# Kernel tuning notes

Measured on AMD Instinct MI355X. Metric: run time of the kernel, lower is better.

## Reference

```python
import jax, jax.numpy as jnp
import numpy as np

N = 50000      # nodes
E = 800000     # edges
F = 500        # num_features
HID = 64       # hidden_channels
H = 4          # num_heads
HC = HID // H  # headc = 16
C = 8          # num_classes
KHOP = 2       # K hops
CST = 1e-5


def setup_inputs() -> dict:
    key = jax.random.key(0)
    ks = jax.random.split(key, 12)
    s = 0.02
    return {
        "node_feat": jax.random.normal(ks[0], (N, F), dtype=jnp.float32),
        "edge_index": jax.random.randint(ks[1], (2, E), 0, N, dtype=jnp.int64),
        "Wi": jax.random.normal(ks[2], (F, HID), dtype=jnp.float32) * s,
        "bi": jnp.zeros((HID,), dtype=jnp.float32),
        "Wq": jax.random.normal(ks[3], (HID, H * HC), dtype=jnp.float32) * s,
        "bq": jnp.zeros((H * HC,), dtype=jnp.float32),
        "Wk": jax.random.normal(ks[4], (HID, H * HC), dtype=jnp.float32) * s,
        "bk": jnp.zeros((H * HC,), dtype=jnp.float32),
        "Wv": jax.random.normal(ks[5], (HID, H * C), dtype=jnp.float32) * s,
        "bv": jnp.zeros((H * C,), dtype=jnp.float32),
        "Wo": jax.random.normal(ks[6], (H * C, C), dtype=jnp.float32) * s,
        "bo": jnp.zeros((C,), dtype=jnp.float32),
        "hopwise": jnp.ones((KHOP + 1,), dtype=jnp.float32),
        "headwise": jnp.zeros((H, KHOP), dtype=jnp.float32),
        "teleport": jnp.ones((1,), dtype=jnp.float32),
    }


def reference(node_feat, edge_index, Wi, bi, Wq, bq, Wk, bk, Wv, bv, Wo, bo,
              hopwise, headwise, teleport):
    row, col = edge_index[0], edge_index[1]
    # degree(col): in-degree; norm = deg^-1 indexed at row (as in the torch code)
    deg = jax.ops.segment_sum(jnp.ones((E,), dtype=node_feat.dtype), col,
                              num_segments=N)
    deg_inv = jnp.where(deg > 0, 1.0 / deg, 0.0)  # [N]

    x = jax.nn.relu(node_feat @ Wi + bi)          # dropout p=0.0 / eval -> identity
    Q = (1.0 + jax.nn.elu(x @ Wq + bq)).reshape(N, H, HC)
    Kf = (1.0 + jax.nn.elu(x @ Wk + bk)).reshape(N, H, HC)
    V = (x @ Wv + bv).reshape(N, H, C)

    M = jnp.einsum('nhi,nhj->nhij', Kf, V)        # [N,H,HC,C]
    hidden = V * hopwise[0]                       # ind_gamma & gamma_softmax
    layerwise = jax.nn.softmax(headwise, axis=0)  # softmax over heads (dim=-2)

    # global attention (teleport) term
    teleportM = jnp.sum(M, axis=0, keepdims=True) / N      # [1,H,HC,C]
    teleportK = jnp.sum(Kf, axis=0, keepdims=True) / N     # [1,H,HC]
    teleportH = jnp.einsum('nhi,bhij->nhj', Q, teleportM)  # [N,H,C]
    teleportC = jnp.einsum('nhi,bhi->nh', Q, teleportK)[..., None] + CST
    teleportH = (teleportH / teleportC).sum(axis=-2)       # [N,C]

    for hop in range(KHOP):
        # norm[e] = deg_inv[row[e]]  =>  pre-scale source nodes, then scatter-add
        M = jax.ops.segment_sum((M * deg_inv[:, None, None, None])[row], col,
                                num_segments=N)
        Kf = jax.ops.segment_sum((Kf * deg_inv[:, None, None])[row], col,
                                 num_segments=N)
        Hh = jnp.einsum('nhi,nhij->nhj', Q, M)             # [N,H,C]
        Cc = jnp.einsum('nhi,nhi->nh', Q, Kf)[..., None] + CST
        gamma = hopwise[hop + 1] * layerwise[:, hop][:, None]  # [H,1]
        hidden = hidden + gamma * (Hh / Cc)

    # multi_concat output projection
    hidden = hidden.reshape(N, H * C) @ Wo + bo
    return hidden + teleport * teleportH
```

## Files before the change

### kernel.cpp

```cpp
#include <hip/hip_runtime.h>
#include <hip/hip_bf16.h>
#include <stdint.h>
#include <stddef.h>

#define NN 50000
#define NE 800000
#define FIN 500
#define HIDN 64
#define NH 4
#define HCD 16
#define NC 8
#define KVROW 192
#define SROW 640
#define CSTF 1e-5f
#define SCAN_NB 196

typedef float f32x2 __attribute__((ext_vector_type(2)));
typedef __attribute__((ext_vector_type(8))) short bf16x8;
typedef __attribute__((ext_vector_type(4))) float f32x4;

__device__ inline float bf_lo(unsigned u) {
    union { unsigned i; float f; } v; v.i = u << 16; return v.f;
}
__device__ inline float bf_hi(unsigned u) {
    union { unsigned i; float f; } v; v.i = u & 0xffff0000u; return v.f;
}
__device__ inline unsigned short f2bf(float f) {
    union { float f; unsigned i; } v; v.f = f;
    unsigned r = v.i + 0x7fffu + ((v.i >> 16) & 1u);
    return (unsigned short)(r >> 16);
}


__global__ void k_deg(const int* __restrict__ col, int* __restrict__ deg) {
    int e = blockIdx.x * blockDim.x + threadIdx.x;
    if (e < NE) atomicAdd(&deg[col[e]], 1);
}

__global__ void k_deginv(const int* __restrict__ deg, float* __restrict__ dinv,
                         int* __restrict__ cursor) {
    int i = blockIdx.x * blockDim.x + threadIdx.x;
    if (i < NN) {
        dinv[i] = deg[i] > 0 ? 1.0f / (float)deg[i] : 0.0f;
        cursor[i] = 0;
    }
}

__global__ void k_bsum(const int* __restrict__ deg, int* __restrict__ bsum) {
    __shared__ int red[256];
    int b = blockIdx.x, t = threadIdx.x;
    int i = b * 256 + t;
    red[t] = (i < NN) ? deg[i] : 0;
    __syncthreads();
    for (int d = 128; d > 0; d >>= 1) {
        if (t < d) red[t] += red[t + d];
        __syncthreads();
    }
    if (t == 0) bsum[b] = red[0];
}

__global__ void k_bscan(const int* __restrict__ bsum, int* __restrict__ bex) {
    __shared__ int s[256];
    int t = threadIdx.x;
    int own = (t < SCAN_NB) ? bsum[t] : 0;
    s[t] = own;
    __syncthreads();
    for (int d = 1; d < 256; d <<= 1) {
        int v = (t >= d) ? s[t - d] : 0;
        __syncthreads();
        s[t] += v;
        __syncthreads();
    }
    if (t < SCAN_NB) bex[t] = s[t] - own;
}

__global__ void k_expand(const int* __restrict__ deg, const int* __restrict__ bex,
                         int* __restrict__ offs) {
    __shared__ int s[256];
    int b = blockIdx.x, t = threadIdx.x;
    int i = b * 256 + t;
    int v = (i < NN) ? deg[i] : 0;
    s[t] = v;
    __syncthreads();
    for (int d = 1; d < 256; d <<= 1) {
        int a = (t >= d) ? s[t - d] : 0;
        __syncthreads();
        s[t] += a;
        __syncthreads();
    }
    int excl = s[t] - v + bex[b];
    if (i < NN) offs[i] = excl;
    if (i == NN - 1) offs[NN] = excl + v;
}

__global__ void k_scatter(const int* __restrict__ row, const int* __restrict__ col,
                          const int* __restrict__ offs, int* __restrict__ cursor,
                          int* __restrict__ csr_src) {
    int e = blockIdx.x * blockDim.x + threadIdx.x;
    if (e < NE) {
        int c = col[e];
        int pos = offs[c] + atomicAdd(&cursor[c], 1);
        csr_src[pos] = row[e];
    }
}


__global__ __launch_bounds__(256) void k_xgemm(const float* __restrict__ nf,
                                               const float* __restrict__ Wi,
                                               const float* __restrict__ bi,
                                               float* __restrict__ x) {
    __shared__ __align__(16) unsigned short a_s[64 * 40];
    __shared__ __align__(16) unsigned short w_s[64 * 40];
    int t = threadIdx.x;
    int lane = t & 63;
    int w = t >> 6;
    int quad = lane >> 4;
    int l15 = lane & 15;
    int n0 = blockIdx.x * 64;

    f32x4 acc[4];
#pragma unroll
    for (int ct = 0; ct < 4; ct++) acc[ct] = (f32x4){0.f, 0.f, 0.f, 0.f};

    for (int k0 = 0; k0 < FIN; k0 += 32) {
        __syncthreads();
#pragma unroll
        for (int p = 0; p < 2; p++) {
            int i = t + p * 256;
            int row = i >> 3;
            int k4 = (i & 7) * 4;
            int kk = k0 + k4;
            int n = n0 + row;
            float4 v = make_float4(0.f, 0.f, 0.f, 0.f);
            if (n < NN && kk < FIN)
                v = *(const float4*)&nf[(size_t)n * FIN + kk];
            unsigned short* d = &a_s[row * 40 + k4];
            d[0] = f2bf(v.x); d[1] = f2bf(v.y); d[2] = f2bf(v.z); d[3] = f2bf(v.w);
        }
#pragma unroll
        for (int p = 0; p < 2; p++) {
            int i = t + p * 256;
            int krow = i >> 4;
            int c4 = (i & 15) * 4;
            int kk = k0 + krow;
            float4 v = make_float4(0.f, 0.f, 0.f, 0.f);
            if (kk < FIN)
                v = *(const float4*)&Wi[(size_t)kk * 64 + c4];
            w_s[(c4 + 0) * 40 + krow] = f2bf(v.x);
            w_s[(c4 + 1) * 40 + krow] = f2bf(v.y);
            w_s[(c4 + 2) * 40 + krow] = f2bf(v.z);
            w_s[(c4 + 3) * 40 + krow] = f2bf(v.w);
        }
        __syncthreads();
        bf16x8 af = *(const bf16x8*)&a_s[(w * 16 + l15) * 40 + quad * 8];
#pragma unroll
        for (int ct = 0; ct < 4; ct++) {
            bf16x8 bf = *(const bf16x8*)&w_s[(ct * 16 + l15) * 40 + quad * 8];
            acc[ct] = __builtin_amdgcn_mfma_f32_16x16x32_bf16(af, bf, acc[ct], 0, 0, 0);
        }
    }
#pragma unroll
    for (int ct = 0; ct < 4; ct++) {
        int c = ct * 16 + l15;
        float bv = bi[c];
#pragma unroll
        for (int r = 0; r < 4; r++) {
            int n = n0 + w * 16 + quad * 4 + r;
            if (n < NN)
                x[(size_t)n * 64 + c] = fmaxf(acc[ct][r] + bv, 0.f);
        }
    }
}


__global__ __launch_bounds__(256) void k_qkv(const float* __restrict__ x,
    const float* __restrict__ Wq, const float* __restrict__ bq,
    const float* __restrict__ Wk, const float* __restrict__ bk,
    const float* __restrict__ Wv, const float* __restrict__ bv,
    const float* __restrict__ hopwise, const float* __restrict__ dinv,
    float* __restrict__ Qg, float* __restrict__ hid,
    unsigned char* __restrict__ kv0, float* __restrict__ tMK) {
    __shared__ float wq_s[64 * 64], wk_s[64 * 64], wv_s[64 * 32];
    __shared__ float bq_s[64], bk_s[64], bv_s[32];
    __shared__ float xs[4][8][64];
    __shared__ float tacc[576];
    int t = threadIdx.x;
    for (int i = t; i < 4096; i += 256) { wq_s[i] = Wq[i]; wk_s[i] = Wk[i]; }
    for (int i = t; i < 2048; i += 256) wv_s[i] = Wv[i];
    if (t < 64) { bq_s[t] = bq[t]; bk_s[t] = bk[t]; }
    if (t >= 64 && t < 96) bv_s[t - 64] = bv[t - 64];
    for (int i = t; i < 576; i += 256) tacc[i] = 0.f;
    __syncthreads();
    int lane = t & 63;
    int w = t >> 6;
    int h = lane >> 4;
    int vcol = lane & 31;
    float hw0 = hopwise[0];
    float tkp = 0.f;
    float tmp_[8];
#pragma unroll
    for (int j = 0; j < 8; j++) tmp_[j] = 0.f;
    int tiles = (NN + 31) >> 5;
    for (int tile = blockIdx.x; tile < tiles; tile += gridDim.x) {
        int n0 = tile * 32 + w * 8;
        __syncthreads();
#pragma unroll
        for (int u = 0; u < 8; u++) {
            int n = n0 + u;
            xs[w][u][lane] = (n < NN) ? x[(size_t)n * 64 + lane] : 0.f;
        }
        __syncthreads();
        float aq[8], ak[8], av[8];
#pragma unroll
        for (int u = 0; u < 8; u++) { aq[u] = 0.f; ak[u] = 0.f; av[u] = 0.f; }
        for (int f = 0; f < 64; f++) {
            float wqv = wq_s[f * 64 + lane];
            float wkv = wk_s[f * 64 + lane];
            float wvv = wv_s[f * 32 + vcol];
#pragma unroll
            for (int u = 0; u < 8; u++) {
                float xf = xs[w][u][f];
                aq[u] = fmaf(xf, wqv, aq[u]);
                ak[u] = fmaf(xf, wkv, ak[u]);
                av[u] = fmaf(xf, wvv, av[u]);
            }
        }
#pragma unroll
        for (int u = 0; u < 8; u++) {
            int n = n0 + u;
            float q = aq[u] + bq_s[lane];
            float k = ak[u] + bk_s[lane];
            float v = av[u] + bv_s[vcol];
            float Qv = q > 0.f ? 1.f + q : expf(q);
            float Kv = k > 0.f ? 1.f + k : expf(k);
            if (n < NN) {
                Qg[(size_t)n * 64 + lane] = Qv;
                float vj[8];
#pragma unroll
                for (int j = 0; j < 8; j++) vj[j] = __shfl(v, h * 8 + j, 64);
                tkp += Kv;
#pragma unroll
                for (int j = 0; j < 8; j++) tmp_[j] += Kv * vj[j];
                float dv = dinv[n];
                unsigned short* kvrow = (unsigned short*)(kv0 + (size_t)n * KVROW);
                kvrow[lane] = f2bf(Kv * dv);
                if (lane < 32) kvrow[64 + lane] = f2bf(v);
                if (lane < 32) hid[(size_t)n * 32 + lane] = v * hw0;
            }
        }
    }
#pragma unroll
    for (int j = 0; j < 8; j++) atomicAdd(&tacc[lane * 8 + j], tmp_[j]);
    atomicAdd(&tacc[512 + lane], tkp);
    __syncthreads();
    for (int i = t; i < 576; i += 256) atomicAdd(&tMK[i], tacc[i]);
}


__global__ __launch_bounds__(256) void k_hop0(const unsigned char* __restrict__ kv0,
    const int* __restrict__ offs, const int* __restrict__ csr_src,
    const float* __restrict__ dinv, const float* __restrict__ Qg,
    const float* __restrict__ hopwise, const float* __restrict__ headwise,
    unsigned char* __restrict__ S1, float* __restrict__ hid) {
    int t = threadIdx.x;
    int lane = t & 63;
    int n = (blockIdx.x * 256 + t) >> 6;
    if (n >= NN) return;
    int h = lane >> 4;
    float e0 = expf(headwise[0 * 2 + 0]);
    float e1 = expf(headwise[1 * 2 + 0]);
    float e2 = expf(headwise[2 * 2 + 0]);
    float e3 = expf(headwise[3 * 2 + 0]);
    float esum = e0 + e1 + e2 + e3;
    float eh = (h == 0) ? e0 : ((h == 1) ? e1 : ((h == 2) ? e2 : e3));
    float gam = hopwise[1] * eh / esum;

    int hoff = 128 + h * 16;
    int o0 = offs[n], o1 = offs[n + 1];
    float kacc = 0.f;
    float4 m0 = make_float4(0.f, 0.f, 0.f, 0.f);
    float4 m1 = make_float4(0.f, 0.f, 0.f, 0.f);
    int e = o0;
    for (; e + 1 < o1; e += 2) {
        int sa = csr_src[e];
        int sb = csr_src[e + 1];
        const unsigned char* ra = kv0 + (size_t)sa * KVROW;
        const unsigned char* rb = kv0 + (size_t)sb * KVROW;
        float ka = bf_lo(((const unsigned short*)ra)[lane]);
        uint4 va = *(const uint4*)(ra + hoff);
        float kb = bf_lo(((const unsigned short*)rb)[lane]);
        uint4 vb = *(const uint4*)(rb + hoff);
        kacc += ka;
        m0.x = fmaf(ka, bf_lo(va.x), m0.x); m0.y = fmaf(ka, bf_hi(va.x), m0.y);
        m0.z = fmaf(ka, bf_lo(va.y), m0.z); m0.w = fmaf(ka, bf_hi(va.y), m0.w);
        m1.x = fmaf(ka, bf_lo(va.z), m1.x); m1.y = fmaf(ka, bf_hi(va.z), m1.y);
        m1.z = fmaf(ka, bf_lo(va.w), m1.z); m1.w = fmaf(ka, bf_hi(va.w), m1.w);
        kacc += kb;
        m0.x = fmaf(kb, bf_lo(vb.x), m0.x); m0.y = fmaf(kb, bf_hi(vb.x), m0.y);
        m0.z = fmaf(kb, bf_lo(vb.y), m0.z); m0.w = fmaf(kb, bf_hi(vb.y), m0.w);
        m1.x = fmaf(kb, bf_lo(vb.z), m1.x); m1.y = fmaf(kb, bf_hi(vb.z), m1.y);
        m1.z = fmaf(kb, bf_lo(vb.w), m1.z); m1.w = fmaf(kb, bf_hi(vb.w), m1.w);
    }
    if (e < o1) {
        int sa = csr_src[e];
        const unsigned char* ra = kv0 + (size_t)sa * KVROW;
        float ka = bf_lo(((const unsigned short*)ra)[lane]);
        uint4 va = *(const uint4*)(ra + hoff);
        kacc += ka;
        m0.x = fmaf(ka, bf_lo(va.x), m0.x); m0.y = fmaf(ka, bf_hi(va.x), m0.y);
        m0.z = fmaf(ka, bf_lo(va.y), m0.z); m0.w = fmaf(ka, bf_hi(va.y), m0.w);
        m1.x = fmaf(ka, bf_lo(va.z), m1.x); m1.y = fmaf(ka, bf_hi(va.z), m1.y);
        m1.z = fmaf(ka, bf_lo(va.w), m1.w); m1.w = fmaf(ka, bf_hi(va.w), m1.w);
    }
    {
        float dv = dinv[n];
        float s16 = dv * 16.f;
        unsigned char* drow = S1 + (size_t)n * SROW;
        ((unsigned short*)drow)[lane] = f2bf(kacc * dv);
        unsigned u0 = __builtin_amdgcn_cvt_pk_fp8_f32(m0.x * s16, m0.y * s16, 0, false);
        u0 = __builtin_amdgcn_cvt_pk_fp8_f32(m0.z * s16, m0.w * s16, u0, true);
        unsigned u1 = __builtin_amdgcn_cvt_pk_fp8_f32(m1.x * s16, m1.y * s16, 0, false);
        u1 = __builtin_amdgcn_cvt_pk_fp8_f32(m1.z * s16, m1.w * s16, u1, true);
        uint2 pv; pv.x = u0; pv.y = u1;
        *(uint2*)(drow + 128 + lane * 8) = pv;
    }
    float qv = Qg[(size_t)n * 64 + lane];
    float hh[8];
    hh[0] = qv * m0.x; hh[1] = qv * m0.y; hh[2] = qv * m0.z; hh[3] = qv * m0.w;
    hh[4] = qv * m1.x; hh[5] = qv * m1.y; hh[6] = qv * m1.z; hh[7] = qv * m1.w;
    float cc = qv * kacc;
#pragma unroll
    for (int s = 1; s < 16; s <<= 1) {
#pragma unroll
        for (int j = 0; j < 8; j++) hh[j] += __shfl_xor(hh[j], s, 16);
        cc += __shfl_xor(cc, s, 16);
    }
    if ((lane & 15) < 8) {
        int j = lane & 7;
        float val = j < 4 ? (j < 2 ? (j == 0 ? hh[0] : hh[1]) : (j == 2 ? hh[2] : hh[3]))
                          : (j < 6 ? (j == 4 ? hh[4] : hh[5]) : (j == 6 ? hh[6] : hh[7]));
        size_t idx = (size_t)n * 32 + h * 8 + j;
        hid[idx] += gam * val / (cc + CSTF);
    }
}


__global__ __launch_bounds__(256) void k_prop1(const unsigned char* __restrict__ Sold,
    const int* __restrict__ offs, const int* __restrict__ csr_src,
    const float* __restrict__ Qg, const float* __restrict__ hopwise,
    const float* __restrict__ headwise, float* __restrict__ hid) {
    int t = threadIdx.x;
    int lane = t & 63;
    int n = (blockIdx.x * 256 + t) >> 6;
    if (n >= NN) return;
    int h = lane >> 4;
    float e0 = expf(headwise[0 * 2 + 1]);
    float e1 = expf(headwise[1 * 2 + 1]);
    float e2 = expf(headwise[2 * 2 + 1]);
    float e3 = expf(headwise[3 * 2 + 1]);
    float esum = e0 + e1 + e2 + e3;
    float eh = (h == 0) ? e0 : ((h == 1) ? e1 : ((h == 2) ? e2 : e3));
    float gam = hopwise[2] * eh / esum * 0.0625f;

    int o0 = offs[n], o1 = offs[n + 1];
    float kacc = 0.f;
    float4 m0 = make_float4(0.f, 0.f, 0.f, 0.f);
    float4 m1 = make_float4(0.f, 0.f, 0.f, 0.f);
    int e = o0;
    for (; e + 1 < o1; e += 2) {
        int sa = csr_src[e];
        int sb = csr_src[e + 1];
        const unsigned char* ra = Sold + (size_t)sa * SROW;
        const unsigned char* rb = Sold + (size_t)sb * SROW;
        float ka = bf_lo(((const unsigned short*)ra)[lane]);
        uint2 mva = *(const uint2*)(ra + 128 + lane * 8);
        float kb = bf_lo(((const unsigned short*)rb)[lane]);
        uint2 mvb = *(const uint2*)(rb + 128 + lane * 8);
        kacc += ka;
        {
            f32x2 a0 = __builtin_amdgcn_cvt_pk_f32_fp8(mva.x, false);
            f32x2 a1 = __builtin_amdgcn_cvt_pk_f32_fp8(mva.x, true);
            f32x2 b0 = __builtin_amdgcn_cvt_pk_f32_fp8(mva.y, false);
            f32x2 b1 = __builtin_amdgcn_cvt_pk_f32_fp8(mva.y, true);
            m0.x += a0.x; m0.y += a0.y; m0.z += a1.x; m0.w += a1.y;
            m1.x += b0.x; m1.y += b0.y; m1.z += b1.x; m1.w += b1.y;
        }
        kacc += kb;
        {
            f32x2 a0 = __builtin_amdgcn_cvt_pk_f32_fp8(mvb.x, false);
            f32x2 a1 = __builtin_amdgcn_cvt_pk_f32_fp8(mvb.x, true);
            f32x2 b0 = __builtin_amdgcn_cvt_pk_f32_fp8(mvb.y, false);
            f32x2 b1 = __builtin_amdgcn_cvt_pk_f32_fp8(mvb.y, true);
            m0.x += a0.x; m0.y += a0.y; m0.z += a1.x; m0.w += a1.y;
            m1.x += b0.x; m1.y += b0.y; m1.z += b1.x; m1.w += b1.y;
        }
    }
    if (e < o1) {
        int sa = csr_src[e];
        const unsigned char* ra = Sold + (size_t)sa * SROW;
        float ka = bf_lo(((const unsigned short*)ra)[lane]);
        uint2 mva = *(const uint2*)(ra + 128 + lane * 8);
        kacc += ka;
        f32x2 a0 = __builtin_amdgcn_cvt_pk_f32_fp8(mva.x, false);
        f32x2 a1 = __builtin_amdgcn_cvt_pk_f32_fp8(mva.x, true);
        f32x2 b0 = __builtin_amdgcn_cvt_pk_f32_fp8(mva.y, false);
        f32x2 b1 = __builtin_amdgcn_cvt_pk_f32_fp8(mva.y, true);
        m0.x += a0.x; m0.y += a0.y; m0.z += a1.x; m0.w += a1.y;
        m1.x += b0.x; m1.y += b0.y; m1.z += b1.x; m1.w += b1.y;
    }
    float qv = Qg[(size_t)n * 64 + lane];
    float hh[8];
    hh[0] = qv * m0.x; hh[1] = qv * m0.y; hh[2] = qv * m0.z; hh[3] = qv * m0.w;
    hh[4] = qv * m1.x; hh[5] = qv * m1.y; hh[6] = qv * m1.z; hh[7] = qv * m1.w;
    float cc = qv * kacc;
#pragma unroll
    for (int s = 1; s < 16; s <<= 1) {
#pragma unroll
        for (int j = 0; j < 8; j++) hh[j] += __shfl_xor(hh[j], s, 16);
        cc += __shfl_xor(cc, s, 16);
    }
    if ((lane & 15) < 8) {
        int j = lane & 7;
        float val = j < 4 ? (j < 2 ? (j == 0 ? hh[0] : hh[1]) : (j == 2 ? hh[2] : hh[3]))
                          : (j < 6 ? (j == 4 ? hh[4] : hh[5]) : (j == 6 ? hh[6] : hh[7]));
        size_t idx = (size_t)n * 32 + h * 8 + j;
        hid[idx] += gam * val / (cc + CSTF);
    }
}


__global__ __launch_bounds__(256) void k_final(const float* __restrict__ hid,
    const float* __restrict__ Qg, const float* __restrict__ Wo,
    const float* __restrict__ bo, const float* __restrict__ tMK,
    const float* __restrict__ teleport, float* __restrict__ out) {
    __shared__ float tm[512];
    __shared__ float tk[64];
    __shared__ float wo[256];
    __shared__ float bos[8];
    int t = threadIdx.x;
    const float invN = 1.0f / (float)NN;
    for (int i = t; i < 512; i += 256) tm[i] = tMK[i] * invN;
    if (t < 64) tk[t] = tMK[512 + t] * invN;
    wo[t] = Wo[t & 255];
    if (t < 8) bos[t] = bo[t];
    __syncthreads();
    float tp = teleport[0];
    int lane = t & 63;
    int sub = lane & 7;
    int g = lane >> 3;
    int wid = (blockIdx.x * 256 + t) >> 6;
    int nwaves = gridDim.x * 4;
    for (int nb = wid * 8; nb < NN; nb += nwaves * 8) {
        int n = nb + g;
        if (n < NN) {
            const float* hrow = hid + (size_t)n * 32;
            const float* qrow = Qg + (size_t)n * 64;
            float o = bos[sub];
#pragma unroll
            for (int m = 0; m < 32; m++) o = fmaf(hrow[m], wo[m * 8 + sub], o);
            float th = 0.f;
#pragma unroll
            for (int h2 = 0; h2 < 4; h2++) {
                float num = 0.f, den = 0.f;
#pragma unroll
                for (int i = 0; i < 16; i++) {
                    float q = qrow[h2 * 16 + i];
                    num = fmaf(q, tm[h2 * 128 + i * 8 + sub], num);
                    den = fmaf(q, tk[h2 * 16 + i], den);
                }
                th += num / (den + CSTF);
            }
            out[(size_t)n * 8 + sub] = o + tp * th;
        }
    }
}


extern "C" void kernel_launch(void* const* d_in, const int* in_sizes, int n_in,
                              void* d_out, int out_size, void* d_ws, size_t ws_size,
                              hipStream_t stream) {
    const float* nf = (const float*)d_in[0];
    const int* ei = (const int*)d_in[1];
    const float* Wi = (const float*)d_in[2];
    const float* bi = (const float*)d_in[3];
    const float* Wq = (const float*)d_in[4];
    const float* bq = (const float*)d_in[5];
    const float* Wk = (const float*)d_in[6];
    const float* bk = (const float*)d_in[7];
    const float* Wv = (const float*)d_in[8];
    const float* bv = (const float*)d_in[9];
    const float* Wo = (const float*)d_in[10];
    const float* bo = (const float*)d_in[11];
    const float* hopwise = (const float*)d_in[12];
    const float* headwise = (const float*)d_in[13];
    const float* teleport = (const float*)d_in[14];
    float* out = (float*)d_out;

    char* base = (char*)d_ws;
    size_t off = 0;
    auto alloc = [&](size_t bytes) -> void* {
        void* p = base + off;
        off = (off + bytes + 255) & ~(size_t)255;
        return p;
    };
    int* deg = (int*)alloc(NN * 4);
    int* cursor = (int*)alloc(NN * 4);
    int* offs = (int*)alloc((NN + 1) * 4);
    int* bsum = (int*)alloc(256 * 4);
    int* bex = (int*)alloc(256 * 4);
    float* dinv = (float*)alloc(NN * 4);
    int* csr_src = (int*)alloc((size_t)NE * 4);
    float* xbuf = (float*)alloc((size_t)NN * 64 * 4);
    float* Qg = (float*)alloc((size_t)NN * 64 * 4);
    float* hid = (float*)alloc((size_t)NN * 32 * 4);
    unsigned char* kv0 = (unsigned char*)alloc((size_t)NN * KVROW);
    unsigned char* S1 = (unsigned char*)alloc((size_t)NN * SROW);
    float* tMK = (float*)alloc(576 * 4);

    const int* rowp = ei;
    const int* colp = ei + NE;

    hipMemsetAsync(deg, 0, NN * 4, stream);
    hipMemsetAsync(tMK, 0, 576 * 4, stream);

    k_deg<<<(NE + 255) / 256, 256, 0, stream>>>(colp, deg);
    k_deginv<<<(NN + 255) / 256, 256, 0, stream>>>(deg, dinv, cursor);
    k_bsum<<<SCAN_NB, 256, 0, stream>>>(deg, bsum);
    k_bscan<<<1, 256, 0, stream>>>(bsum, bex);
    k_expand<<<SCAN_NB, 256, 0, stream>>>(deg, bex, offs);
    k_scatter<<<(NE + 255) / 256, 256, 0, stream>>>(rowp, colp, offs, cursor, csr_src);
    k_xgemm<<<(NN + 63) / 64, 256, 0, stream>>>(nf, Wi, bi, xbuf);
    k_qkv<<<512, 256, 0, stream>>>(xbuf, Wq, bq, Wk, bk, Wv, bv, hopwise, dinv,
                                   Qg, hid, kv0, tMK);
    k_hop0<<<(NN * 64 + 255) / 256, 256, 0, stream>>>(kv0, offs, csr_src, dinv, Qg,
                                                      hopwise, headwise, S1, hid);
    k_prop1<<<(NN * 64 + 255) / 256, 256, 0, stream>>>(S1, offs, csr_src, Qg,
                                                       hopwise, headwise, hid);
    k_final<<<1563, 256, 0, stream>>>(hid, Qg, Wo, bo, tMK, teleport, out);
}
```

Baseline: 491.3 us.

## Persist Wi in LDS for xgemm, unroll gather loops by four, fold tMK memset

The input GEMM becomes a persistent kernel on 512 blocks. Each block loads the whole bf16 weight matrix once into XOR-swizzled shared memory and reads node features straight from global memory into MFMA fragments, which removes the per-k-step staging and barriers. The hop0 and prop1 gather loops are unrolled from two to four edges so more independent loads are in flight, and the tMK memset is folded into k_deginv. Risks are lower occupancy from the 64KB of LDS per block and higher register pressure in the gather loops; the rewrite also fixes an m1.z accumulator typo in the hop0 tail.

```diff
diff --git a/kernel.cpp b/kernel.cpp
--- a/kernel.cpp
+++ b/kernel.cpp
@@ -14,6 +14,7 @@
 #define SROW 640
 #define CSTF 1e-5f
 #define SCAN_NB 196
+#define NTILES 782
 
 typedef float f32x2 __attribute__((ext_vector_type(2)));
 typedef __attribute__((ext_vector_type(8))) short bf16x8;
@@ -30,6 +31,10 @@
     unsigned r = v.i + 0x7fffu + ((v.i >> 16) & 1u);
     return (unsigned short)(r >> 16);
 }
+__device__ inline unsigned pack2bf(float a, float b) {
+    __hip_bfloat162 h = __float22bfloat162_rn(make_float2(a, b));
+    unsigned r; __builtin_memcpy(&r, &h, 4); return r;
+}
 
 
 __global__ void k_deg(const int* __restrict__ col, int* __restrict__ deg) {
@@ -38,12 +43,14 @@
 }
 
 __global__ void k_deginv(const int* __restrict__ deg, float* __restrict__ dinv,
-                         int* __restrict__ cursor) {
+                         int* __restrict__ cursor, float* __restrict__ tMK) {
     int i = blockIdx.x * blockDim.x + threadIdx.x;
     if (i < NN) {
         dinv[i] = deg[i] > 0 ? 1.0f / (float)deg[i] : 0.0f;
         cursor[i] = 0;
     }
+    if (blockIdx.x == 0)
+        for (int j = threadIdx.x; j < 576; j += 256) tMK[j] = 0.f;
 }
 
 __global__ void k_bsum(const int* __restrict__ deg, int* __restrict__ bsum) {
@@ -109,65 +116,66 @@
                                                const float* __restrict__ Wi,
                                                const float* __restrict__ bi,
                                                float* __restrict__ x) {
-    __shared__ __align__(16) unsigned short a_s[64 * 40];
-    __shared__ __align__(16) unsigned short w_s[64 * 40];
+    __shared__ unsigned short w_s[64 * 512];
     int t = threadIdx.x;
+    for (int i = t; i < 8192; i += 256) {
+        int kk = i >> 4;
+        int c4 = (i & 15) * 4;
+        float4 v = make_float4(0.f, 0.f, 0.f, 0.f);
+        if (kk < FIN) v = *(const float4*)&Wi[(size_t)kk * 64 + c4];
+        int kb = kk >> 3, kj = kk & 7;
+#pragma unroll
+        for (int j = 0; j < 4; j++) {
+            int c = c4 + j;
+            float val = (j == 0) ? v.x : (j == 1) ? v.y : (j == 2) ? v.z : v.w;
+            w_s[c * 512 + ((kb ^ (c & 7)) << 3) + kj] = f2bf(val);
+        }
+    }
+    __syncthreads();
+
     int lane = t & 63;
     int w = t >> 6;
     int quad = lane >> 4;
     int l15 = lane & 15;
-    int n0 = blockIdx.x * 64;
-
-    f32x4 acc[4];
-#pragma unroll
-    for (int ct = 0; ct < 4; ct++) acc[ct] = (f32x4){0.f, 0.f, 0.f, 0.f};
-
-    for (int k0 = 0; k0 < FIN; k0 += 32) {
-        __syncthreads();
-#pragma unroll
-        for (int p = 0; p < 2; p++) {
-            int i = t + p * 256;
-            int row = i >> 3;
-            int k4 = (i & 7) * 4;
-            int kk = k0 + k4;
-            int n = n0 + row;
-            float4 v = make_float4(0.f, 0.f, 0.f, 0.f);
-            if (n < NN && kk < FIN)
-                v = *(const float4*)&nf[(size_t)n * FIN + kk];
-            unsigned short* d = &a_s[row * 40 + k4];
-            d[0] = f2bf(v.x); d[1] = f2bf(v.y); d[2] = f2bf(v.z); d[3] = f2bf(v.w);
-        }
-#pragma unroll
-        for (int p = 0; p < 2; p++) {
-            int i = t + p * 256;
-            int krow = i >> 4;
-            int c4 = (i & 15) * 4;
-            int kk = k0 + krow;
-            float4 v = make_float4(0.f, 0.f, 0.f, 0.f);
-            if (kk < FIN)
-                v = *(const float4*)&Wi[(size_t)kk * 64 + c4];
-            w_s[(c4 + 0) * 40 + krow] = f2bf(v.x);
-            w_s[(c4 + 1) * 40 + krow] = f2bf(v.y);
-            w_s[(c4 + 2) * 40 + krow] = f2bf(v.z);
-            w_s[(c4 + 3) * 40 + krow] = f2bf(v.w);
-        }
-        __syncthreads();
-        bf16x8 af = *(const bf16x8*)&a_s[(w * 16 + l15) * 40 + quad * 8];
+
+    for (int tile = blockIdx.x; tile < NTILES; tile += gridDim.x) {
+        int n0 = tile * 64;
+        int rown = n0 + w * 16 + l15;
+        const float* arow = &nf[(size_t)(rown < NN ? rown : 0) * FIN];
+
+        f32x4 acc[4];
+#pragma unroll
+        for (int ct = 0; ct < 4; ct++) acc[ct] = (f32x4){0.f, 0.f, 0.f, 0.f};
+
+        for (int k0 = 0; k0 < 512; k0 += 32) {
+            int kk = k0 + quad * 8;
+            float4 a0 = make_float4(0.f, 0.f, 0.f, 0.f);
+            float4 a1 = make_float4(0.f, 0.f, 0.f, 0.f);
+            if (kk < FIN) a0 = *(const float4*)&arow[kk];
+            if (kk + 4 < FIN) a1 = *(const float4*)&arow[kk + 4];
+            union { unsigned u[4]; bf16x8 v; } A;
+            A.u[0] = pack2bf(a0.x, a0.y);
+            A.u[1] = pack2bf(a0.z, a0.w);
+            A.u[2] = pack2bf(a1.x, a1.y);
+            A.u[3] = pack2bf(a1.z, a1.w);
+            int kb = kk >> 3;
+#pragma unroll
+            for (int ct = 0; ct < 4; ct++) {
+                int c = ct * 16 + l15;
+                bf16x8 bfr = *(const bf16x8*)&w_s[c * 512 + ((kb ^ (c & 7)) << 3)];
+                acc[ct] = __builtin_amdgcn_mfma_f32_16x16x32_bf16(A.v, bfr, acc[ct], 0, 0, 0);
+            }
+        }
 #pragma unroll
         for (int ct = 0; ct < 4; ct++) {
-            bf16x8 bf = *(const bf16x8*)&w_s[(ct * 16 + l15) * 40 + quad * 8];
-            acc[ct] = __builtin_amdgcn_mfma_f32_16x16x32_bf16(af, bf, acc[ct], 0, 0, 0);
-        }
-    }
-#pragma unroll
-    for (int ct = 0; ct < 4; ct++) {
-        int c = ct * 16 + l15;
-        float bv = bi[c];
-#pragma unroll
-        for (int r = 0; r < 4; r++) {
-            int n = n0 + w * 16 + quad * 4 + r;
-            if (n < NN)
-                x[(size_t)n * 64 + c] = fmaxf(acc[ct][r] + bv, 0.f);
+            int c = ct * 16 + l15;
+            float bv = bi[c];
+#pragma unroll
+            for (int r = 0; r < 4; r++) {
+                int n = n0 + w * 16 + quad * 4 + r;
+                if (n < NN)
+                    x[(size_t)n * 64 + c] = fmaxf(acc[ct][r] + bv, 0.f);
+            }
         }
     }
 }
@@ -267,10 +275,10 @@
     int n = (blockIdx.x * 256 + t) >> 6;
     if (n >= NN) return;
     int h = lane >> 4;
-    float e0 = expf(headwise[0 * 2 + 0]);
-    float e1 = expf(headwise[1 * 2 + 0]);
-    float e2 = expf(headwise[2 * 2 + 0]);
-    float e3 = expf(headwise[3 * 2 + 0]);
+    float e0 = expf(headwise[0]);
+    float e1 = expf(headwise[2]);
+    float e2 = expf(headwise[4]);
+    float e3 = expf(headwise[6]);
     float esum = e0 + e1 + e2 + e3;
     float eh = (h == 0) ? e0 : ((h == 1) ? e1 : ((h == 2) ? e2 : e3));
     float gam = hopwise[1] * eh / esum;
@@ -281,36 +289,35 @@
     float4 m0 = make_float4(0.f, 0.f, 0.f, 0.f);
     float4 m1 = make_float4(0.f, 0.f, 0.f, 0.f);
     int e = o0;
-    for (; e + 1 < o1; e += 2) {
-        int sa = csr_src[e];
-        int sb = csr_src[e + 1];
-        const unsigned char* ra = kv0 + (size_t)sa * KVROW;
-        const unsigned char* rb = kv0 + (size_t)sb * KVROW;
-        float ka = bf_lo(((const unsigned short*)ra)[lane]);
-        uint4 va = *(const uint4*)(ra + hoff);
-        float kb = bf_lo(((const unsigned short*)rb)[lane]);
-        uint4 vb = *(const uint4*)(rb + hoff);
+    for (; e + 3 < o1; e += 4) {
+        float kk_[4]; uint4 vv[4];
+#pragma unroll
+        for (int q = 0; q < 4; q++) {
+            int s = csr_src[e + q];
+            const unsigned char* r = kv0 + (size_t)s * KVROW;
+            kk_[q] = bf_lo(((const unsigned short*)r)[lane]);
+            vv[q] = *(const uint4*)(r + hoff);
+        }
+#pragma unroll
+        for (int q = 0; q < 4; q++) {
+            float ka = kk_[q]; uint4 va = vv[q];
+            kacc += ka;
+            m0.x = fmaf(ka, bf_lo(va.x), m0.x); m0.y = fmaf(ka, bf_hi(va.x), m0.y);
+            m0.z = fmaf(ka, bf_lo(va.y), m0.z); m0.w = fmaf(ka, bf_hi(va.y), m0.w);
+            m1.x = fmaf(ka, bf_lo(va.z), m1.x); m1.y = fmaf(ka, bf_hi(va.z), m1.y);
+            m1.z = fmaf(ka, bf_lo(va.w), m1.z); m1.w = fmaf(ka, bf_hi(va.w), m1.w);
+        }
+    }
+    for (; e < o1; e++) {
+        int s = csr_src[e];
+        const unsigned char* r = kv0 + (size_t)s * KVROW;
+        float ka = bf_lo(((const unsigned short*)r)[lane]);
+        uint4 va = *(const uint4*)(r + hoff);
         kacc += ka;
         m0.x = fmaf(ka, bf_lo(va.x), m0.x); m0.y = fmaf(ka, bf_hi(va.x), m0.y);
         m0.z = fmaf(ka, bf_lo(va.y), m0.z); m0.w = fmaf(ka, bf_hi(va.y), m0.w);
         m1.x = fmaf(ka, bf_lo(va.z), m1.x); m1.y = fmaf(ka, bf_hi(va.z), m1.y);
         m1.z = fmaf(ka, bf_lo(va.w), m1.z); m1.w = fmaf(ka, bf_hi(va.w), m1.w);
-        kacc += kb;
-        m0.x = fmaf(kb, bf_lo(vb.x), m0.x); m0.y = fmaf(kb, bf_hi(vb.x), m0.y);
-        m0.z = fmaf(kb, bf_lo(vb.y), m0.z); m0.w = fmaf(kb, bf_hi(vb.y), m0.w);
-        m1.x = fmaf(kb, bf_lo(vb.z), m1.x); m1.y = fmaf(kb, bf_hi(vb.z), m1.y);
-        m1.z = fmaf(kb, bf_lo(vb.w), m1.z); m1.w = fmaf(kb, bf_hi(vb.w), m1.w);
-    }
-    if (e < o1) {
-        int sa = csr_src[e];
-        const unsigned char* ra = kv0 + (size_t)sa * KVROW;
-        float ka = bf_lo(((const unsigned short*)ra)[lane]);
-        uint4 va = *(const uint4*)(ra + hoff);
-        kacc += ka;
-        m0.x = fmaf(ka, bf_lo(va.x), m0.x); m0.y = fmaf(ka, bf_hi(va.x), m0.y);
-        m0.z = fmaf(ka, bf_lo(va.y), m0.z); m0.w = fmaf(ka, bf_hi(va.y), m0.w);
-        m1.x = fmaf(ka, bf_lo(va.z), m1.x); m1.y = fmaf(ka, bf_hi(va.z), m1.y);
-        m1.z = fmaf(ka, bf_lo(va.w), m1.w); m1.w = fmaf(ka, bf_hi(va.w), m1.w);
     }
     {
         float dv = dinv[n];
@@ -354,10 +361,10 @@
     int n = (blockIdx.x * 256 + t) >> 6;
     if (n >= NN) return;
     int h = lane >> 4;
-    float e0 = expf(headwise[0 * 2 + 1]);
-    float e1 = expf(headwise[1 * 2 + 1]);
-    float e2 = expf(headwise[2 * 2 + 1]);
-    float e3 = expf(headwise[3 * 2 + 1]);
+    float e0 = expf(headwise[1]);
+    float e1 = expf(headwise[3]);
+    float e2 = expf(headwise[5]);
+    float e3 = expf(headwise[7]);
     float esum = e0 + e1 + e2 + e3;
     float eh = (h == 0) ? e0 : ((h == 1) ? e1 : ((h == 2) ? e2 : e3));
     float gam = hopwise[2] * eh / esum * 0.0625f;
@@ -367,39 +374,31 @@
     float4 m0 = make_float4(0.f, 0.f, 0.f, 0.f);
     float4 m1 = make_float4(0.f, 0.f, 0.f, 0.f);
     int e = o0;
-    for (; e + 1 < o1; e += 2) {
-        int sa = csr_src[e];
-        int sb = csr_src[e + 1];
-        const unsigned char* ra = Sold + (size_t)sa * SROW;
-        const unsigned char* rb = Sold + (size_t)sb * SROW;
-        float ka = bf_lo(((const unsigned short*)ra)[lane]);
-        uint2 mva = *(const uint2*)(ra + 128 + lane * 8);
-        float kb = bf_lo(((const unsigned short*)rb)[lane]);
-        uint2 mvb = *(const uint2*)(rb + 128 + lane * 8);
-        kacc += ka;
-        {
-            f32x2 a0 = __builtin_amdgcn_cvt_pk_f32_fp8(mva.x, false);
-            f32x2 a1 = __builtin_amdgcn_cvt_pk_f32_fp8(mva.x, true);
-            f32x2 b0 = __builtin_amdgcn_cvt_pk_f32_fp8(mva.y, false);
-            f32x2 b1 = __builtin_amdgcn_cvt_pk_f32_fp8(mva.y, true);
+    for (; e + 3 < o1; e += 4) {
+        float kk_[4]; uint2 mv[4];
+#pragma unroll
+        for (int q = 0; q < 4; q++) {
+            int s = csr_src[e + q];
+            const unsigned char* r = Sold + (size_t)s * SROW;
+            kk_[q] = bf_lo(((const unsigned short*)r)[lane]);
+            mv[q] = *(const uint2*)(r + 128 + lane * 8);
+        }
+#pragma unroll
+        for (int q = 0; q < 4; q++) {
+            kacc += kk_[q];
+            f32x2 a0 = __builtin_amdgcn_cvt_pk_f32_fp8(mv[q].x, false);
+            f32x2 a1 = __builtin_amdgcn_cvt_pk_f32_fp8(mv[q].x, true);
+            f32x2 b0 = __builtin_amdgcn_cvt_pk_f32_fp8(mv[q].y, false);
+            f32x2 b1 = __builtin_amdgcn_cvt_pk_f32_fp8(mv[q].y, true);
             m0.x += a0.x; m0.y += a0.y; m0.z += a1.x; m0.w += a1.y;
             m1.x += b0.x; m1.y += b0.y; m1.z += b1.x; m1.w += b1.y;
         }
-        kacc += kb;
-        {
-            f32x2 a0 = __builtin_amdgcn_cvt_pk_f32_fp8(mvb.x, false);
-            f32x2 a1 = __builtin_amdgcn_cvt_pk_f32_fp8(mvb.x, true);
-            f32x2 b0 = __builtin_amdgcn_cvt_pk_f32_fp8(mvb.y, false);
-            f32x2 b1 = __builtin_amdgcn_cvt_pk_f32_fp8(mvb.y, true);
-            m0.x += a0.x; m0.y += a0.y; m0.z += a1.x; m0.w += a1.y;
-            m1.x += b0.x; m1.y += b0.y; m1.z += b1.x; m1.w += b1.y;
-        }
-    }
-    if (e < o1) {
-        int sa = csr_src[e];
-        const unsigned char* ra = Sold + (size_t)sa * SROW;
-        float ka = bf_lo(((const unsigned short*)ra)[lane]);
-        uint2 mva = *(const uint2*)(ra + 128 + lane * 8);
+    }
+    for (; e < o1; e++) {
+        int s = csr_src[e];
+        const unsigned char* r = Sold + (size_t)s * SROW;
+        float ka = bf_lo(((const unsigned short*)r)[lane]);
+        uint2 mva = *(const uint2*)(r + 128 + lane * 8);
         kacc += ka;
         f32x2 a0 = __builtin_amdgcn_cvt_pk_f32_fp8(mva.x, false);
         f32x2 a1 = __builtin_amdgcn_cvt_pk_f32_fp8(mva.x, true);
@@ -521,15 +520,14 @@
     const int* colp = ei + NE;
 
     hipMemsetAsync(deg, 0, NN * 4, stream);
-    hipMemsetAsync(tMK, 0, 576 * 4, stream);
 
     k_deg<<<(NE + 255) / 256, 256, 0, stream>>>(colp, deg);
-    k_deginv<<<(NN + 255) / 256, 256, 0, stream>>>(deg, dinv, cursor);
+    k_deginv<<<(NN + 255) / 256, 256, 0, stream>>>(deg, dinv, cursor, tMK);
     k_bsum<<<SCAN_NB, 256, 0, stream>>>(deg, bsum);
     k_bscan<<<1, 256, 0, stream>>>(bsum, bex);
     k_expand<<<SCAN_NB, 256, 0, stream>>>(deg, bex, offs);
     k_scatter<<<(NE + 255) / 256, 256, 0, stream>>>(rowp, colp, offs, cursor, csr_src);
-    k_xgemm<<<(NN + 63) / 64, 256, 0, stream>>>(nf, Wi, bi, xbuf);
+    k_xgemm<<<512, 256, 0, stream>>>(nf, Wi, bi, xbuf);
     k_qkv<<<512, 256, 0, stream>>>(xbuf, Wq, bq, Wk, bk, Wv, bv, hopwise, dinv,
                                    Qg, hid, kv0, tMK);
     k_hop0<<<(NN * 64 + 255) / 256, 256, 0, stream>>>(kv0, offs, csr_src, dinv, Qg,
```

Measured after the change: 495.3 us. Within noise of the previous version (+0.8%).
